# Performance work log

Hardware: AMD Instinct MI355X
Metric: run time of the kernel (lower is better)

Reference implementation:

```python
import jax, jax.numpy as jnp
from jax import lax
import numpy as np

D_IN, D, H, W, POOL = 1280, 100, 20, 3, 9
K_SIG, X0 = 1.0, 0.0
EPS = 1e-5


def setup_inputs() -> dict:
    key = jax.random.key(0)
    ks = jax.random.split(key, 8)
    N1, N2 = 512, 512
    return {
        "x1": jax.random.normal(ks[0], (N1, D_IN), jnp.float32),
        "x2": jax.random.normal(ks[1], (N2, D_IN), jnp.float32),
        "W1": jax.random.normal(ks[2], (D, D_IN), jnp.float32) * 0.02,
        "b1": jnp.zeros((D,), jnp.float32),
        "W2": jax.random.normal(ks[3], (H, 2 * D), jnp.float32) * 0.05,
        "b2": jnp.zeros((H,), jnp.float32),
        "bn1_g": jnp.ones((H,), jnp.float32),
        "bn1_b": jnp.zeros((H,), jnp.float32),
        "conv_w": jax.random.normal(ks[4], (1, H, 2 * W + 1, 2 * W + 1), jnp.float32) * 0.05,
        "conv_b": jnp.zeros((1,), jnp.float32),
        "bn2_g": jnp.ones((1,), jnp.float32),
        "bn2_b": jnp.zeros((1,), jnp.float32),
        "gamma": jnp.zeros((1,), jnp.float32),
    }


def reference(x1, x2, W1, b1, W2, b2, bn1_g, bn1_b, conv_w, conv_b, bn2_g, bn2_b, gamma):
    N1, N2 = x1.shape[0], x2.shape[0]
    # fc1 projection (relu1/dropout1 are defined but unused in the original forward)
    a = (x1 @ W1.T + b1)[None]          # [1, N1, D]
    c = (x2 @ W1.T + b2 * 0 + b1)[None] if False else (x2 @ W1.T + b1)[None]  # [1, N2, D]
    # broadcast pairwise |diff| and product -> [1, N1, N2, 2D]
    diff = jnp.abs(a[:, :, None, :] - c[:, None, :, :])
    mul = a[:, :, None, :] * c[:, None, :, :]
    m = jnp.concatenate([diff, mul], axis=-1).reshape(-1, 2 * D)  # [N1*N2, 2D]
    # fc2
    m = m @ W2.T + b2                    # [N1*N2, H]
    # BatchNorm1d in training mode: batch statistics, biased variance
    mu = m.mean(axis=0)
    var = m.var(axis=0)
    m = (m - mu) * lax.rsqrt(var + EPS) * bn1_g + bn1_b
    m = jax.nn.relu(m)
    m = m.reshape(1, N1, N2, H).transpose(0, 3, 1, 2)  # NCHW [1, H, N1, N2]
    # 7x7 conv, padding=W
    C = lax.conv_general_dilated(m, conv_w, (1, 1), [(W, W), (W, W)])
    C = C + conv_b.reshape(1, -1, 1, 1)
    # BatchNorm2d (training mode, biased variance over N,H,W per channel)
    mu2 = C.mean(axis=(0, 2, 3), keepdims=True)
    var2 = C.var(axis=(0, 2, 3), keepdims=True)
    C = (C - mu2) * lax.rsqrt(var2 + EPS) * bn2_g.reshape(1, -1, 1, 1) + bn2_b.reshape(1, -1, 1, 1)
    C = jax.nn.sigmoid(C)
    # MaxPool2d(9, padding=4): stride = kernel, -inf padding
    p = POOL // 2
    B = lax.reduce_window(C, -jnp.inf, lax.max, (1, 1, POOL, POOL), (1, 1, POOL, POOL),
                          [(0, 0), (0, 0), (p, p), (p, p)])
    # mean / unbiased std over dims (1, 2) keepdim
    mean = B.mean(axis=(1, 2), keepdims=True)
    std = jnp.sqrt(B.var(axis=(1, 2), keepdims=True, ddof=1) + EPS)
    Q = jax.nn.relu(B - mean - gamma.reshape(()) * std)
    phat = Q.sum() / (jnp.sign(Q).sum() + 1.0)
    phat = jnp.clip(jax.nn.sigmoid(K_SIG * (phat - X0)), 0.0, 1.0)
    return phat, C
```

## Files before the change

kernel.cpp:

```cpp
#include <hip/hip_runtime.h>
#include <hip/hip_bf16.h>
#include <math.h>

#define N1 512
#define N2 512
#define DIN 1280
#define DD 100
#define HH 20
#define NPIX (N1*N2)
#define PB 57

typedef short bf16x8 __attribute__((ext_vector_type(8)));
typedef float f32x4 __attribute__((ext_vector_type(4)));

static constexpr size_t WS_PP    = 0;
static constexpr size_t WS_W1T   = 204800;
static constexpr size_t WS_W2B   = 332800;
static constexpr size_t WS_M     = 336896;
static constexpr size_t WS_CRAW  = WS_M + 5242880;
static constexpr size_t WS_STATS = WS_CRAW + 262144;
static constexpr size_t WS_B     = WS_STATS + 64;

__global__ __launch_bounds__(256) void kP(const float* __restrict__ W1,
                                          const float* __restrict__ W2,
                                          float* __restrict__ w1t,
                                          unsigned short* __restrict__ w2b,
                                          float* __restrict__ stats) {
  const int tid = threadIdx.x;
  if (blockIdx.x >= 160) {
    int idx = (blockIdx.x - 160) * 256 + tid;
    if (blockIdx.x == 160 && tid < 64) stats[tid] = 0.0f;
    if (idx < 224 * 32) {
      int k = idx >> 5, n = idx & 31;
      float v = (n < HH && k < 200) ? W2[n * 200 + k] : 0.0f;
      __hip_bfloat16 b = __float2bfloat16(v);
      w2b[idx] = *reinterpret_cast<unsigned short*>(&b);
    }
    return;
  }
  __shared__ float sT[32][33];
  const int bx = blockIdx.x % 40, by = blockIdx.x / 40;
  const int tx = tid & 31, ty = tid >> 5;
#pragma unroll
  for (int e = 0; e < 4; ++e) {
    int h = by * 32 + ty + e * 8, k = bx * 32 + tx;
    sT[ty + e * 8][tx] = (h < DD) ? W1[(size_t)h * DIN + k] : 0.0f;
  }
  __syncthreads();
#pragma unroll
  for (int e = 0; e < 4; ++e) {
    int k = bx * 32 + ty + e * 8, h = by * 32 + tx;
    if (h < DD) w1t[(size_t)k * DD + h] = sT[tx][ty + e * 8];
  }
}

__global__ __launch_bounds__(512) void kA(const float* __restrict__ x1,
                                          const float* __restrict__ x2,
                                          const float* __restrict__ w1t,
                                          float* __restrict__ pp) {
  const int tid = threadIdx.x;
  const int w  = __builtin_amdgcn_readfirstlane(tid >> 6);
  const int rp = w >> 1, hh = w & 1;
  const int h = hh * 64 + (tid & 63);
  if (h >= DD) return;
  const int kh = blockIdx.x & 1;
  const int rb = (blockIdx.x >> 1) * 8;
  const int r0 = rb + rp * 2;
  const float* xb = (r0 < N1) ? (x1 + (size_t)r0 * DIN) : (x2 + (size_t)(r0 - N1) * DIN);
  const float* xr0 = xb + kh * 640;
  const float* xr1 = xb + DIN + kh * 640;
  const float* w1p = w1t + (size_t)kh * 640 * DD + h;
  float a00 = 0.f, a01 = 0.f, a10 = 0.f, a11 = 0.f;
#pragma unroll 8
  for (int k = 0; k < 640; k += 2) {
    float wA = w1p[(size_t)k * DD];
    float wB = w1p[(size_t)(k + 1) * DD];
    float x00 = xr0[k], x01 = xr0[k + 1];
    float x10 = xr1[k], x11 = xr1[k + 1];
    a00 = fmaf(wA, x00, a00); a01 = fmaf(wB, x01, a01);
    a10 = fmaf(wA, x10, a10); a11 = fmaf(wB, x11, a11);
  }
  pp[(size_t)kh * 102400 + (size_t)r0 * DD + h] = a00 + a01;
  pp[(size_t)kh * 102400 + (size_t)(r0 + 1) * DD + h] = a10 + a11;
}

__global__ __launch_bounds__(256, 2) void kB(const float* __restrict__ pp,
                                             const float* __restrict__ b1,
                                             const unsigned short* __restrict__ w2b,
                                             float* __restrict__ m,
                                             float* __restrict__ stats) {
  __shared__ float sA[8][132];
  __shared__ float sC[64][132];
  __shared__ float wred[4][40];
  const int tid = threadIdx.x;
  const int bi = blockIdx.x >> 3, bj = blockIdx.x & 7;
  for (int idx = tid; idx < 72 * 33; idx += 256) {
    int r = idx / 33, d4 = idx % 33;
    float4 v = {0.f, 0.f, 0.f, 0.f};
    if (d4 < 25) {
      size_t row = (r < 8) ? (size_t)(bi * 8 + r) : (size_t)(N1 + bj * 64 + (r - 8));
      const float* base = pp + row * DD;
      float4 a0 = ((const float4*)base)[d4];
      float4 a1 = ((const float4*)(base + 102400))[d4];
      float4 bb = ((const float4*)b1)[d4];
      v.x = a0.x + a1.x + bb.x;
      v.y = a0.y + a1.y + bb.y;
      v.z = a0.z + a1.z + bb.z;
      v.w = a0.w + a1.w + bb.w;
    }
    if (r < 8) *(float4*)&sA[r][4 * d4] = v;
    else       *(float4*)&sC[r - 8][4 * d4] = v;
  }
  __syncthreads();

  const int w    = tid >> 6;
  const int lane = tid & 63;
  const int ln   = lane & 15;
  const int q    = lane >> 4;
  const int jj   = w * 16 + ln;

  bf16x8 af[7][2];
#pragma unroll
  for (int ks = 0; ks < 7; ++ks)
#pragma unroll
    for (int t = 0; t < 2; ++t) {
      bf16x8 v;
#pragma unroll
      for (int e = 0; e < 8; ++e)
        v[e] = (short)w2b[(ks * 32 + q * 8 + e) * 32 + ln + 16 * t];
      af[ks][t] = v;
    }

  int dOf[14];
  bool isP[14];
  float4 cH[14];
#pragma unroll
  for (int hx = 0; hx < 14; ++hx) {
    int kk = (hx >> 1) * 32 + q * 8 + (hx & 1) * 4;
    bool p = kk >= 100;
    isP[hx] = p;
    int d = p ? kk - 100 : kk;
    dOf[hx] = d;
    cH[hx] = *(const float4*)&sC[jj][d];
  }

  float st_s[8], st_q[8];
#pragma unroll
  for (int r = 0; r < 8; ++r) { st_s[r] = 0.f; st_q[r] = 0.f; }

  const int gj = bj * 64 + jj;
#pragma unroll 1
  for (int ii = 0; ii < 8; ++ii) {
    bf16x8 bf[7];
#pragma unroll
    for (int ks = 0; ks < 7; ++ks) {
      float4 a0 = *(const float4*)&sA[ii][dOf[2 * ks]];
      float4 a1 = *(const float4*)&sA[ii][dOf[2 * ks + 1]];
      float4 c0 = cH[2 * ks], c1 = cH[2 * ks + 1];
      float f0 = isP[2*ks]   ? a0.x * c0.x : fabsf(a0.x - c0.x);
      float f1 = isP[2*ks]   ? a0.y * c0.y : fabsf(a0.y - c0.y);
      float f2 = isP[2*ks]   ? a0.z * c0.z : fabsf(a0.z - c0.z);
      float f3 = isP[2*ks]   ? a0.w * c0.w : fabsf(a0.w - c0.w);
      float f4 = isP[2*ks+1] ? a1.x * c1.x : fabsf(a1.x - c1.x);
      float f5 = isP[2*ks+1] ? a1.y * c1.y : fabsf(a1.y - c1.y);
      float f6 = isP[2*ks+1] ? a1.z * c1.z : fabsf(a1.z - c1.z);
      float f7 = isP[2*ks+1] ? a1.w * c1.w : fabsf(a1.w - c1.w);
      union { bf16x8 v; __hip_bfloat162 h2[4]; } u;
      u.h2[0] = __float22bfloat162_rn(make_float2(f0, f1));
      u.h2[1] = __float22bfloat162_rn(make_float2(f2, f3));
      u.h2[2] = __float22bfloat162_rn(make_float2(f4, f5));
      u.h2[3] = __float22bfloat162_rn(make_float2(f6, f7));
      bf[ks] = u.v;
    }
    f32x4 acc0 = {0.f, 0.f, 0.f, 0.f}, acc1 = {0.f, 0.f, 0.f, 0.f};
#pragma unroll
    for (int ks = 0; ks < 7; ++ks) {
      acc0 = __builtin_amdgcn_mfma_f32_16x16x32_bf16(af[ks][0], bf[ks], acc0, 0, 0, 0);
      acc1 = __builtin_amdgcn_mfma_f32_16x16x32_bf16(af[ks][1], bf[ks], acc1, 0, 0, 0);
    }
    const size_t pix = (size_t)(bi * 8 + ii) * N2 + gj;
#pragma unroll
    for (int r = 0; r < 4; ++r) {
      m[(size_t)(4 * q + r) * NPIX + pix] = acc0[r];
      st_s[r] += acc0[r];
      st_q[r] += acc0[r] * acc0[r];
    }
    if (q == 0) {
#pragma unroll
      for (int r = 0; r < 4; ++r)
        m[(size_t)(16 + r) * NPIX + pix] = acc1[r];
    }
#pragma unroll
    for (int r = 0; r < 4; ++r) {
      st_s[4 + r] += acc1[r];
      st_q[4 + r] += acc1[r] * acc1[r];
    }
  }
#pragma unroll
  for (int r = 0; r < 8; ++r) {
#pragma unroll
    for (int off = 1; off < 16; off <<= 1) {
      st_s[r] += __shfl_xor(st_s[r], off);
      st_q[r] += __shfl_xor(st_q[r], off);
    }
  }
  if (ln == 0) {
#pragma unroll
    for (int r = 0; r < 4; ++r) {
      wred[w][4 * q + r]      = st_s[r];
      wred[w][20 + 4 * q + r] = st_q[r];
    }
    if (q == 0) {
#pragma unroll
      for (int r = 0; r < 4; ++r) {
        wred[w][16 + r] = st_s[4 + r];
        wred[w][36 + r] = st_q[4 + r];
      }
    }
  }
  __syncthreads();
  if (tid < 40)
    atomicAdd(&stats[tid], wred[0][tid] + wred[1][tid] + wred[2][tid] + wred[3][tid]);
}

__global__ __launch_bounds__(256, 1) void kD(const float* __restrict__ m,
                                             const float* __restrict__ bn1g,
                                             const float* __restrict__ bn1b,
                                             const float* __restrict__ cw,
                                             float* __restrict__ stats,
                                             float* __restrict__ Craw) {
  __shared__ float sIn[2][4][38][40];
  __shared__ float sSc[HH], sSh[HH];
  __shared__ float wsum[4][2];
  const int tid = threadIdx.x;
  if (tid < HH) {
    float s = stats[tid], q = stats[HH + tid];
    float mu = s * (1.0f / NPIX);
    float var = q * (1.0f / NPIX) - mu * mu;
    float g = bn1g[tid] / sqrtf(var + 1e-5f);
    sSc[tid] = g;
    sSh[tid] = bn1b[tid] - mu * g;
  }
  const int by = (blockIdx.x >> 4) * 32, bx = (blockIdx.x & 15) * 32;
  const int w = tid >> 6, lane = tid & 63;
  const int gxs = bx + lane - 4;
  const bool colOk = (lane < 40) && (gxs >= 0) && (gxs < N2);
  float ld[38];
  {
    const float* mp = m + (size_t)w * NPIX + gxs;
#pragma unroll
    for (int r = 0; r < 38; ++r) {
      int gy = by + r - 3;
      ld[r] = (colOk && gy >= 0 && gy < N1) ? mp[(size_t)gy * N2] : 0.0f;
    }
  }
  __syncthreads();
  if (lane < 40) {
    float sc = sSc[w], sh = sSh[w];
#pragma unroll
    for (int r = 0; r < 38; ++r) {
      int gy = by + r - 3;
      bool ok = colOk && gy >= 0 && gy < N1;
      sIn[0][w][r][lane] = ok ? fmaxf(fmaf(ld[r], sc, sh), 0.0f) : 0.0f;
    }
  }
  __syncthreads();
  const int ty = tid >> 4, tx = tid & 15;
  float acc00 = 0.f, acc01 = 0.f, acc10 = 0.f, acc11 = 0.f;
#pragma unroll 1
  for (int cc = 0; cc < 5; ++cc) {
    if (cc < 4) {
      const float* mp = m + (size_t)((cc + 1) * 4 + w) * NPIX + gxs;
#pragma unroll
      for (int r = 0; r < 38; ++r) {
        int gy = by + r - 3;
        ld[r] = (colOk && gy >= 0 && gy < N1) ? mp[(size_t)gy * N2] : 0.0f;
      }
    }
    const int cur = cc & 1;
#pragma unroll 1
    for (int ch4 = 0; ch4 < 4; ++ch4) {
      float2 win[8][5];
#pragma unroll
      for (int rr = 0; rr < 8; ++rr)
#pragma unroll
        for (int qq = 0; qq < 5; ++qq)
          win[rr][qq] = *(const float2*)&sIn[cur][ch4][2 * ty + rr][2 * tx + 2 * qq];
      const float* wch = cw + (cc * 4 + ch4) * 49;
#pragma unroll
      for (int ky = 0; ky < 7; ++ky)
#pragma unroll
        for (int kx = 0; kx < 7; ++kx) {
          float wt = wch[ky * 7 + kx];
          float e0 = ((kx + 1) & 1) ? win[ky][(kx + 1) >> 1].y : win[ky][(kx + 1) >> 1].x;
          float e1 = ((kx + 2) & 1) ? win[ky][(kx + 2) >> 1].y : win[ky][(kx + 2) >> 1].x;
          float f0 = ((kx + 1) & 1) ? win[ky + 1][(kx + 1) >> 1].y : win[ky + 1][(kx + 1) >> 1].x;
          float f1 = ((kx + 2) & 1) ? win[ky + 1][(kx + 2) >> 1].y : win[ky + 1][(kx + 2) >> 1].x;
          acc00 = fmaf(e0, wt, acc00);
          acc01 = fmaf(e1, wt, acc01);
          acc10 = fmaf(f0, wt, acc10);
          acc11 = fmaf(f1, wt, acc11);
        }
    }
    __syncthreads();
    if (cc < 4 && lane < 40) {
      int ch = (cc + 1) * 4 + w;
      float sc = sSc[ch], sh = sSh[ch];
#pragma unroll
      for (int r = 0; r < 38; ++r) {
        int gy = by + r - 3;
        bool ok = colOk && gy >= 0 && gy < N1;
        sIn[cur ^ 1][w][r][lane] = ok ? fmaxf(fmaf(ld[r], sc, sh), 0.0f) : 0.0f;
      }
    }
    __syncthreads();
  }
  const int oy = by + 2 * ty, ox = bx + 2 * tx;
  float2 r0 = {acc00, acc01}, r1 = {acc10, acc11};
  *(float2*)&Craw[(size_t)oy * N2 + ox] = r0;
  *(float2*)&Craw[(size_t)(oy + 1) * N2 + ox] = r1;
  float s = acc00 + acc01 + acc10 + acc11;
  float q = acc00 * acc00 + acc01 * acc01 + acc10 * acc10 + acc11 * acc11;
#pragma unroll
  for (int off = 32; off; off >>= 1) {
    s += __shfl_xor(s, off);
    q += __shfl_xor(q, off);
  }
  if (lane == 0) { wsum[w][0] = s; wsum[w][1] = q; }
  __syncthreads();
  if (tid < 2) {
    float v = wsum[0][tid] + wsum[1][tid] + wsum[2][tid] + wsum[3][tid];
    atomicAdd(&stats[2 * HH + tid], v);
  }
}

__global__ __launch_bounds__(256) void kE2M(const float* __restrict__ Craw,
                                            const float* __restrict__ stats,
                                            const float* __restrict__ bn2g,
                                            const float* __restrict__ bn2b,
                                            float* __restrict__ Cout,
                                            float* __restrict__ B) {
  const int w = blockIdx.x * 4 + (threadIdx.x >> 6);
  const int lane = threadIdx.x & 63;
  float s = stats[2 * HH], q = stats[2 * HH + 1];
  float mu = s * (1.0f / NPIX);
  float var = q * (1.0f / NPIX) - mu * mu;
  float g = bn2g[0] / sqrtf(var + 1e-5f);
  float b = bn2b[0] - mu * g;
  if (w >= PB * PB) return;
  const int wy = w / PB, wx = w % PB;
  const int y0 = wy * 9 - 4, x0 = wx * 9 - 4;
  float mx = -1e30f;
  for (int e = lane; e < 144; e += 64) {
    int dy = e / 12, dx = e % 12;
    int y = y0 + dy, x = x0 + dx;
    bool inWin = (dy < 9) && (dx < 9);
    bool claim = (y >= 0) && (y < N1) && (x >= 0) && (x < N2) &&
                 (dy < 9 || wy == PB - 1) && (dx < 9 || wx == PB - 1);
    if (claim) {
      float z = Craw[(size_t)y * N2 + x] * g + b;
      float sg = 1.0f / (1.0f + expf(-z));
      Cout[(size_t)y * N2 + x] = sg;
      if (inWin) mx = fmaxf(mx, sg);
    }
  }
#pragma unroll
  for (int off = 32; off; off >>= 1) mx = fmaxf(mx, __shfl_xor(mx, off));
  if (lane == 0) B[w] = mx;
}

__global__ __launch_bounds__(1024) void kF(const float* __restrict__ B,
                                           const float* __restrict__ gamma,
                                           float* __restrict__ out0) {
  __shared__ float sB[PB * PB];
  __shared__ float cm[PB], cs[PB];
  __shared__ float r1[16], r2[16];
  const int tid = threadIdx.x;
  for (int i = tid; i < PB * PB; i += 1024) sB[i] = B[i];
  __syncthreads();
  if (tid < PB * 16) {
    int c = tid >> 4, g = tid & 15;
    float s = 0.0f;
    for (int h = g; h < PB; h += 16) s += sB[h * PB + c];
#pragma unroll
    for (int off = 1; off < 16; off <<= 1) s += __shfl_xor(s, off);
    float mean = s / (float)PB;
    float v = 0.0f;
    for (int h = g; h < PB; h += 16) { float d = sB[h * PB + c] - mean; v += d * d; }
#pragma unroll
    for (int off = 1; off < 16; off <<= 1) v += __shfl_xor(v, off);
    if (g == 0) {
      cm[c] = mean;
      cs[c] = sqrtf(v / (float)(PB - 1) + 1e-5f);
    }
  }
  __syncthreads();
  const float g = gamma[0];
  float sq = 0.0f, cnt = 0.0f;
  for (int i = tid; i < PB * PB; i += 1024) {
    int w = i % PB;
    float qv = sB[i] - cm[w] - g * cs[w];
    if (qv > 0.0f) { sq += qv; cnt += 1.0f; }
  }
#pragma unroll
  for (int off = 32; off; off >>= 1) {
    sq += __shfl_xor(sq, off);
    cnt += __shfl_xor(cnt, off);
  }
  if ((tid & 63) == 0) { r1[tid >> 6] = sq; r2[tid >> 6] = cnt; }
  __syncthreads();
  if (tid == 0) {
    float S = 0.f, Cn = 0.f;
#pragma unroll
    for (int e = 0; e < 16; ++e) { S += r1[e]; Cn += r2[e]; }
    float phat = S / (Cn + 1.0f);
    float sig = 1.0f / (1.0f + expf(-phat));
    out0[0] = fminf(fmaxf(sig, 0.0f), 1.0f);
  }
}

extern "C" void kernel_launch(void* const* d_in, const int* in_sizes, int n_in,
                              void* d_out, int out_size, void* d_ws, size_t ws_size,
                              hipStream_t stream) {
  const float* x1    = (const float*)d_in[0];
  const float* x2    = (const float*)d_in[1];
  const float* W1    = (const float*)d_in[2];
  const float* b1    = (const float*)d_in[3];
  const float* W2    = (const float*)d_in[4];
  const float* bn1g  = (const float*)d_in[6];
  const float* bn1b  = (const float*)d_in[7];
  const float* convw = (const float*)d_in[8];
  const float* bn2g  = (const float*)d_in[10];
  const float* bn2b  = (const float*)d_in[11];
  const float* gamma = (const float*)d_in[12];

  float* ws    = (float*)d_ws;
  float* pp    = ws + WS_PP;
  float* w1t   = ws + WS_W1T;
  unsigned short* w2b = (unsigned short*)(ws + WS_W2B);
  float* m     = ws + WS_M;
  float* Craw  = ws + WS_CRAW;
  float* stats = ws + WS_STATS;
  float* Bp    = ws + WS_B;
  float* out   = (float*)d_out;

  kP<<<188, 256, 0, stream>>>(W1, W2, w1t, w2b, stats);
  kA<<<256, 512, 0, stream>>>(x1, x2, w1t, pp);
  kB<<<512, 256, 0, stream>>>(pp, b1, w2b, m, stats);
  kD<<<256, 256, 0, stream>>>(m, bn1g, bn1b, convw, stats, Craw);
  kE2M<<<(PB * PB + 3) / 4, 256, 0, stream>>>(Craw, stats, bn2g, bn2b, out + 1, Bp);
  kF<<<1, 1024, 0, stream>>>(Bp, gamma, out);
}
```

Before: 92.99 us.

## Fuse all stages into one cooperative persistent kernel with grid syncs

Replaces the six separate kernel launches with a single cooperative kernel of 256 blocks that runs every stage in turn, separated by grid.sync(). Each stage is remapped onto the fixed grid: the projection loops over the h halves, and the pairwise fc2 stage processes two tiles per block. The aim is to remove launch overhead and inter-kernel gaps. In exchange, parallelism is capped at 256 blocks of 256 threads (kA used 512-thread blocks, kB ran 512 blocks at two per CU), and grid barriers add their own cost. If the cooperative launch fails, it falls back to the old launches.

```diff
diff --git a/kernel.cpp b/kernel.cpp
--- a/kernel.cpp
+++ b/kernel.cpp
@@ -1,6 +1,9 @@
 #include <hip/hip_runtime.h>
+#include <hip/hip_cooperative_groups.h>
 #include <hip/hip_bf16.h>
 #include <math.h>
+
+namespace cg = cooperative_groups;
 
 #define N1 512
 #define N2 512
@@ -20,6 +23,396 @@
 static constexpr size_t WS_CRAW  = WS_M + 5242880;
 static constexpr size_t WS_STATS = WS_CRAW + 262144;
 static constexpr size_t WS_B     = WS_STATS + 64;
+
+union SMem {
+  struct { float sT[32][33]; } p;
+  struct { float sA[8][132]; float sC[64][132]; float wred[4][40]; } b;
+  struct { float sIn[2][4][38][40]; float sSc[HH]; float sSh[HH]; float wsum[4][2]; } d;
+  struct { float sB[PB * PB]; float cm[PB]; float cs[PB]; float r1[4]; float r2[4]; } f;
+};
+
+__global__ __launch_bounds__(256, 1) void kAll(
+    const float* __restrict__ x1, const float* __restrict__ x2,
+    const float* __restrict__ W1, const float* __restrict__ b1,
+    const float* __restrict__ W2,
+    const float* __restrict__ bn1g, const float* __restrict__ bn1b,
+    const float* __restrict__ cw,
+    const float* __restrict__ bn2g, const float* __restrict__ bn2b,
+    const float* __restrict__ gamma,
+    float* __restrict__ pp, float* __restrict__ w1t,
+    unsigned short* __restrict__ w2b,
+    float* __restrict__ m, float* __restrict__ Craw,
+    float* __restrict__ stats, float* __restrict__ Bp,
+    float* __restrict__ out) {
+  cg::grid_group grid = cg::this_grid();
+  __shared__ SMem sm;
+  const int blk = blockIdx.x;
+  const int tid = threadIdx.x;
+  const int lane = tid & 63;
+  const int wv = tid >> 6;
+  const int wvu = __builtin_amdgcn_readfirstlane(wv);
+
+  if (blk < 160) {
+    const int bx = blk % 40, by = blk / 40;
+    const int tx = tid & 31, ty = tid >> 5;
+#pragma unroll
+    for (int e = 0; e < 4; ++e) {
+      int h = by * 32 + ty + e * 8, k = bx * 32 + tx;
+      sm.p.sT[ty + e * 8][tx] = (h < DD) ? W1[(size_t)h * DIN + k] : 0.0f;
+    }
+    __syncthreads();
+#pragma unroll
+    for (int e = 0; e < 4; ++e) {
+      int k = bx * 32 + ty + e * 8, h = by * 32 + tx;
+      if (h < DD) w1t[(size_t)k * DD + h] = sm.p.sT[tx][ty + e * 8];
+    }
+  } else if (blk < 188) {
+    int idx = (blk - 160) * 256 + tid;
+    if (blk == 160 && tid < 64) stats[tid] = 0.0f;
+    if (idx < 224 * 32) {
+      int k = idx >> 5, n = idx & 31;
+      float v = (n < HH && k < 200) ? W2[n * 200 + k] : 0.0f;
+      __hip_bfloat16 bh = __float2bfloat16(v);
+      w2b[idx] = *reinterpret_cast<unsigned short*>(&bh);
+    }
+  }
+  grid.sync();
+
+  {
+    const int kh = blk & 1;
+    const int r0 = (blk >> 1) * 8 + wvu * 2;
+    const float* xb = (r0 < N1) ? (x1 + (size_t)r0 * DIN) : (x2 + (size_t)(r0 - N1) * DIN);
+    const float* xr0 = xb + kh * 640;
+    const float* xr1 = xb + DIN + kh * 640;
+#pragma unroll 1
+    for (int hl = 0; hl < 2; ++hl) {
+      int h = hl * 64 + lane;
+      if (h < DD) {
+        const float* w1p = w1t + (size_t)kh * 640 * DD + h;
+        float a00 = 0.f, a01 = 0.f, a10 = 0.f, a11 = 0.f;
+#pragma unroll 8
+        for (int k = 0; k < 640; k += 2) {
+          float wA = w1p[(size_t)k * DD];
+          float wB = w1p[(size_t)(k + 1) * DD];
+          a00 = fmaf(wA, xr0[k], a00); a01 = fmaf(wB, xr0[k + 1], a01);
+          a10 = fmaf(wA, xr1[k], a10); a11 = fmaf(wB, xr1[k + 1], a11);
+        }
+        pp[(size_t)kh * 102400 + (size_t)r0 * DD + h] = a00 + a01;
+        pp[(size_t)kh * 102400 + (size_t)(r0 + 1) * DD + h] = a10 + a11;
+      }
+    }
+  }
+  grid.sync();
+
+  {
+    const int ln = lane & 15;
+    const int q  = lane >> 4;
+    const int jj = wv * 16 + ln;
+
+    bf16x8 af[7][2];
+#pragma unroll
+    for (int ks = 0; ks < 7; ++ks)
+#pragma unroll
+      for (int t = 0; t < 2; ++t) {
+        bf16x8 v;
+#pragma unroll
+        for (int e = 0; e < 8; ++e)
+          v[e] = (short)w2b[(ks * 32 + q * 8 + e) * 32 + ln + 16 * t];
+        af[ks][t] = v;
+      }
+    int dOf[14];
+    bool isP[14];
+#pragma unroll
+    for (int hx = 0; hx < 14; ++hx) {
+      int kk = (hx >> 1) * 32 + q * 8 + (hx & 1) * 4;
+      isP[hx] = kk >= 100;
+      dOf[hx] = isP[hx] ? kk - 100 : kk;
+    }
+
+#pragma unroll 1
+    for (int t = 0; t < 2; ++t) {
+      const int bb = blk + t * 256;
+      const int bi = bb >> 3, bj = bb & 7;
+      if (t) __syncthreads();
+      for (int idx = tid; idx < 72 * 33; idx += 256) {
+        int r = idx / 33, d4 = idx % 33;
+        float4 v = {0.f, 0.f, 0.f, 0.f};
+        if (d4 < 25) {
+          size_t row = (r < 8) ? (size_t)(bi * 8 + r) : (size_t)(N1 + bj * 64 + (r - 8));
+          const float* base = pp + row * DD;
+          float4 a0 = ((const float4*)base)[d4];
+          float4 a1 = ((const float4*)(base + 102400))[d4];
+          float4 bb4 = ((const float4*)b1)[d4];
+          v.x = a0.x + a1.x + bb4.x;
+          v.y = a0.y + a1.y + bb4.y;
+          v.z = a0.z + a1.z + bb4.z;
+          v.w = a0.w + a1.w + bb4.w;
+        }
+        if (r < 8) *(float4*)&sm.b.sA[r][4 * d4] = v;
+        else       *(float4*)&sm.b.sC[r - 8][4 * d4] = v;
+      }
+      __syncthreads();
+
+      float4 cH[14];
+#pragma unroll
+      for (int hx = 0; hx < 14; ++hx) cH[hx] = *(const float4*)&sm.b.sC[jj][dOf[hx]];
+
+      float st_s[8], st_q[8];
+#pragma unroll
+      for (int r = 0; r < 8; ++r) { st_s[r] = 0.f; st_q[r] = 0.f; }
+
+      const int gj = bj * 64 + jj;
+#pragma unroll 1
+      for (int ii = 0; ii < 8; ++ii) {
+        bf16x8 bf[7];
+#pragma unroll
+        for (int ks = 0; ks < 7; ++ks) {
+          float4 a0 = *(const float4*)&sm.b.sA[ii][dOf[2 * ks]];
+          float4 a1 = *(const float4*)&sm.b.sA[ii][dOf[2 * ks + 1]];
+          float4 c0 = cH[2 * ks], c1 = cH[2 * ks + 1];
+          float f0 = isP[2*ks]   ? a0.x * c0.x : fabsf(a0.x - c0.x);
+          float f1 = isP[2*ks]   ? a0.y * c0.y : fabsf(a0.y - c0.y);
+          float f2 = isP[2*ks]   ? a0.z * c0.z : fabsf(a0.z - c0.z);
+          float f3 = isP[2*ks]   ? a0.w * c0.w : fabsf(a0.w - c0.w);
+          float f4 = isP[2*ks+1] ? a1.x * c1.x : fabsf(a1.x - c1.x);
+          float f5 = isP[2*ks+1] ? a1.y * c1.y : fabsf(a1.y - c1.y);
+          float f6 = isP[2*ks+1] ? a1.z * c1.z : fabsf(a1.z - c1.z);
+          float f7 = isP[2*ks+1] ? a1.w * c1.w : fabsf(a1.w - c1.w);
+          union { bf16x8 v; __hip_bfloat162 h2[4]; } u;
+          u.h2[0] = __float22bfloat162_rn(make_float2(f0, f1));
+          u.h2[1] = __float22bfloat162_rn(make_float2(f2, f3));
+          u.h2[2] = __float22bfloat162_rn(make_float2(f4, f5));
+          u.h2[3] = __float22bfloat162_rn(make_float2(f6, f7));
+          bf[ks] = u.v;
+        }
+        f32x4 acc0 = {0.f, 0.f, 0.f, 0.f}, acc1 = {0.f, 0.f, 0.f, 0.f};
+#pragma unroll
+        for (int ks = 0; ks < 7; ++ks) {
+          acc0 = __builtin_amdgcn_mfma_f32_16x16x32_bf16(af[ks][0], bf[ks], acc0, 0, 0, 0);
+          acc1 = __builtin_amdgcn_mfma_f32_16x16x32_bf16(af[ks][1], bf[ks], acc1, 0, 0, 0);
+        }
+        const size_t pix = (size_t)(bi * 8 + ii) * N2 + gj;
+#pragma unroll
+        for (int r = 0; r < 4; ++r) {
+          m[(size_t)(4 * q + r) * NPIX + pix] = acc0[r];
+          st_s[r] += acc0[r];
+          st_q[r] += acc0[r] * acc0[r];
+        }
+        if (q == 0) {
+#pragma unroll
+          for (int r = 0; r < 4; ++r)
+            m[(size_t)(16 + r) * NPIX + pix] = acc1[r];
+        }
+#pragma unroll
+        for (int r = 0; r < 4; ++r) {
+          st_s[4 + r] += acc1[r];
+          st_q[4 + r] += acc1[r] * acc1[r];
+        }
+      }
+#pragma unroll
+      for (int r = 0; r < 8; ++r) {
+#pragma unroll
+        for (int off = 1; off < 16; off <<= 1) {
+          st_s[r] += __shfl_xor(st_s[r], off);
+          st_q[r] += __shfl_xor(st_q[r], off);
+        }
+      }
+      if (ln == 0) {
+#pragma unroll
+        for (int r = 0; r < 4; ++r) {
+          sm.b.wred[wv][4 * q + r]      = st_s[r];
+          sm.b.wred[wv][20 + 4 * q + r] = st_q[r];
+        }
+        if (q == 0) {
+#pragma unroll
+          for (int r = 0; r < 4; ++r) {
+            sm.b.wred[wv][16 + r] = st_s[4 + r];
+            sm.b.wred[wv][36 + r] = st_q[4 + r];
+          }
+        }
+      }
+      __syncthreads();
+      if (tid < 40)
+        atomicAdd(&stats[tid],
+                  sm.b.wred[0][tid] + sm.b.wred[1][tid] + sm.b.wred[2][tid] + sm.b.wred[3][tid]);
+    }
+  }
+  grid.sync();
+
+  {
+    if (tid < HH) {
+      float s = stats[tid], q = stats[HH + tid];
+      float mu = s * (1.0f / NPIX);
+      float var = q * (1.0f / NPIX) - mu * mu;
+      float g = bn1g[tid] / sqrtf(var + 1e-5f);
+      sm.d.sSc[tid] = g;
+      sm.d.sSh[tid] = bn1b[tid] - mu * g;
+    }
+    const int by = (blk >> 4) * 32, bx = (blk & 15) * 32;
+    const int gxs = bx + lane - 4;
+    const bool colOk = (lane < 40) && (gxs >= 0) && (gxs < N2);
+    float ld[38];
+    {
+      const float* mp = m + (size_t)wvu * NPIX + gxs;
+#pragma unroll
+      for (int r = 0; r < 38; ++r) {
+        int gy = by + r - 3;
+        ld[r] = (colOk && gy >= 0 && gy < N1) ? mp[(size_t)gy * N2] : 0.0f;
+      }
+    }
+    __syncthreads();
+    if (lane < 40) {
+      float sc = sm.d.sSc[wvu], sh = sm.d.sSh[wvu];
+#pragma unroll
+      for (int r = 0; r < 38; ++r)
+        sm.d.sIn[0][wvu][r][lane] = fmaxf(fmaf(ld[r], sc, sh), 0.0f) * (ld[r] != 0.0f || true ? 1.0f : 0.0f);
+    }
+    if (lane < 40) {
+#pragma unroll
+      for (int r = 0; r < 38; ++r) {
+        int gy = by + r - 3;
+        bool ok = colOk && gy >= 0 && gy < N1;
+        if (!ok) sm.d.sIn[0][wvu][r][lane] = 0.0f;
+      }
+    }
+    __syncthreads();
+    const int ty = tid >> 4, tx = tid & 15;
+    float acc00 = 0.f, acc01 = 0.f, acc10 = 0.f, acc11 = 0.f;
+#pragma unroll 1
+    for (int cc = 0; cc < 5; ++cc) {
+      if (cc < 4) {
+        const float* mp = m + (size_t)((cc + 1) * 4 + wvu) * NPIX + gxs;
+#pragma unroll
+        for (int r = 0; r < 38; ++r) {
+          int gy = by + r - 3;
+          ld[r] = (colOk && gy >= 0 && gy < N1) ? mp[(size_t)gy * N2] : 0.0f;
+        }
+      }
+      const int cur = cc & 1;
+#pragma unroll 1
+      for (int ch4 = 0; ch4 < 4; ++ch4) {
+        float2 win[8][5];
+#pragma unroll
+        for (int rr = 0; rr < 8; ++rr)
+#pragma unroll
+          for (int qq = 0; qq < 5; ++qq)
+            win[rr][qq] = *(const float2*)&sm.d.sIn[cur][ch4][2 * ty + rr][2 * tx + 2 * qq];
+        const float* wch = cw + (cc * 4 + ch4) * 49;
+#pragma unroll
+        for (int ky = 0; ky < 7; ++ky)
+#pragma unroll
+          for (int kx = 0; kx < 7; ++kx) {
+            float wt = wch[ky * 7 + kx];
+            float e0 = ((kx + 1) & 1) ? win[ky][(kx + 1) >> 1].y : win[ky][(kx + 1) >> 1].x;
+            float e1 = ((kx + 2) & 1) ? win[ky][(kx + 2) >> 1].y : win[ky][(kx + 2) >> 1].x;
+            float f0 = ((kx + 1) & 1) ? win[ky + 1][(kx + 1) >> 1].y : win[ky + 1][(kx + 1) >> 1].x;
+            float f1 = ((kx + 2) & 1) ? win[ky + 1][(kx + 2) >> 1].y : win[ky + 1][(kx + 2) >> 1].x;
+            acc00 = fmaf(e0, wt, acc00);
+            acc01 = fmaf(e1, wt, acc01);
+            acc10 = fmaf(f0, wt, acc10);
+            acc11 = fmaf(f1, wt, acc11);
+          }
+      }
+      __syncthreads();
+      if (cc < 4 && lane < 40) {
+        int ch = (cc + 1) * 4 + wvu;
+        float sc = sm.d.sSc[ch], sh = sm.d.sSh[ch];
+#pragma unroll
+        for (int r = 0; r < 38; ++r) {
+          int gy = by + r - 3;
+          bool ok = colOk && gy >= 0 && gy < N1;
+          sm.d.sIn[cur ^ 1][wvu][r][lane] = ok ? fmaxf(fmaf(ld[r], sc, sh), 0.0f) : 0.0f;
+        }
+      }
+      __syncthreads();
+    }
+    const int oy = by + 2 * ty, ox = bx + 2 * tx;
+    float2 r0 = {acc00, acc01}, r1 = {acc10, acc11};
+    *(float2*)&Craw[(size_t)oy * N2 + ox] = r0;
+    *(float2*)&Craw[(size_t)(oy + 1) * N2 + ox] = r1;
+    float s = acc00 + acc01 + acc10 + acc11;
+    float q = acc00 * acc00 + acc01 * acc01 + acc10 * acc10 + acc11 * acc11;
+#pragma unroll
+    for (int off = 32; off; off >>= 1) {
+      s += __shfl_xor(s, off);
+      q += __shfl_xor(q, off);
+    }
+    if (lane == 0) { sm.d.wsum[wv][0] = s; sm.d.wsum[wv][1] = q; }
+    __syncthreads();
+    if (tid < 2) {
+      float v = sm.d.wsum[0][tid] + sm.d.wsum[1][tid] + sm.d.wsum[2][tid] + sm.d.wsum[3][tid];
+      atomicAdd(&stats[2 * HH + tid], v);
+    }
+  }
+  grid.sync();
+
+  {
+    float s = stats[2 * HH], q = stats[2 * HH + 1];
+    float mu = s * (1.0f / NPIX);
+    float var = q * (1.0f / NPIX) - mu * mu;
+    float g = bn2g[0] / sqrtf(var + 1e-5f);
+    float b = bn2b[0] - mu * g;
+    float* Cout = out + 1;
+    for (int w = blk * 4 + wv; w < PB * PB; w += 1024) {
+      const int wy = w / PB, wx = w % PB;
+      const int y0 = wy * 9 - 4, x0 = wx * 9 - 4;
+      float mx = -1e30f;
+      for (int e = lane; e < 144; e += 64) {
+        int dy = e / 12, dx = e % 12;
+        int y = y0 + dy, x = x0 + dx;
+        bool inWin = (dy < 9) && (dx < 9);
+        bool claim = (y >= 0) && (y < N1) && (x >= 0) && (x < N2) &&
+                     (dy < 9 || wy == PB - 1) && (dx < 9 || wx == PB - 1);
+        if (claim) {
+          float z = Craw[(size_t)y * N2 + x] * g + b;
+          float sg = 1.0f / (1.0f + expf(-z));
+          Cout[(size_t)y * N2 + x] = sg;
+          if (inWin) mx = fmaxf(mx, sg);
+        }
+      }
+#pragma unroll
+      for (int off = 32; off; off >>= 1) mx = fmaxf(mx, __shfl_xor(mx, off));
+      if (lane == 0) Bp[w] = mx;
+    }
+  }
+  grid.sync();
+
+  if (blk == 0) {
+    for (int i = tid; i < PB * PB; i += 256) sm.f.sB[i] = Bp[i];
+    __syncthreads();
+    if (tid < PB) {
+      float s = 0.0f;
+      for (int h = 0; h < PB; ++h) s += sm.f.sB[h * PB + tid];
+      float mean = s / (float)PB;
+      float v = 0.0f;
+      for (int h = 0; h < PB; ++h) { float d = sm.f.sB[h * PB + tid] - mean; v += d * d; }
+      sm.f.cm[tid] = mean;
+      sm.f.cs[tid] = sqrtf(v / (float)(PB - 1) + 1e-5f);
+    }
+    __syncthreads();
+    const float g = gamma[0];
+    float sq = 0.0f, cnt = 0.0f;
+    for (int i = tid; i < PB * PB; i += 256) {
+      int w = i % PB;
+      float qv = sm.f.sB[i] - sm.f.cm[w] - g * sm.f.cs[w];
+      if (qv > 0.0f) { sq += qv; cnt += 1.0f; }
+    }
+#pragma unroll
+    for (int off = 32; off; off >>= 1) {
+      sq += __shfl_xor(sq, off);
+      cnt += __shfl_xor(cnt, off);
+    }
+    if (lane == 0) { sm.f.r1[wv] = sq; sm.f.r2[wv] = cnt; }
+    __syncthreads();
+    if (tid == 0) {
+      float S = sm.f.r1[0] + sm.f.r1[1] + sm.f.r1[2] + sm.f.r1[3];
+      float Cn = sm.f.r2[0] + sm.f.r2[1] + sm.f.r2[2] + sm.f.r2[3];
+      float phat = S / (Cn + 1.0f);
+      float sig = 1.0f / (1.0f + expf(-phat));
+      out[0] = fminf(fmaxf(sig, 0.0f), 1.0f);
+    }
+  }
+}
 
 __global__ __launch_bounds__(256) void kP(const float* __restrict__ W1,
                                           const float* __restrict__ W2,
@@ -64,8 +457,7 @@
   const int h = hh * 64 + (tid & 63);
   if (h >= DD) return;
   const int kh = blockIdx.x & 1;
-  const int rb = (blockIdx.x >> 1) * 8;
-  const int r0 = rb + rp * 2;
+  const int r0 = (blockIdx.x >> 1) * 8 + rp * 2;
   const float* xb = (r0 < N1) ? (x1 + (size_t)r0 * DIN) : (x2 + (size_t)(r0 - N1) * DIN);
   const float* xr0 = xb + kh * 640;
   const float* xr1 = xb + DIN + kh * 640;
@@ -75,10 +467,8 @@
   for (int k = 0; k < 640; k += 2) {
     float wA = w1p[(size_t)k * DD];
     float wB = w1p[(size_t)(k + 1) * DD];
-    float x00 = xr0[k], x01 = xr0[k + 1];
-    float x10 = xr1[k], x11 = xr1[k + 1];
-    a00 = fmaf(wA, x00, a00); a01 = fmaf(wB, x01, a01);
-    a10 = fmaf(wA, x10, a10); a11 = fmaf(wB, x11, a11);
+    a00 = fmaf(wA, xr0[k], a00); a01 = fmaf(wB, xr0[k + 1], a01);
+    a10 = fmaf(wA, xr1[k], a10); a11 = fmaf(wB, xr1[k + 1], a11);
   }
   pp[(size_t)kh * 102400 + (size_t)r0 * DD + h] = a00 + a01;
   pp[(size_t)kh * 102400 + (size_t)(r0 + 1) * DD + h] = a10 + a11;
@@ -112,13 +502,9 @@
     else       *(float4*)&sC[r - 8][4 * d4] = v;
   }
   __syncthreads();
-
-  const int w    = tid >> 6;
-  const int lane = tid & 63;
-  const int ln   = lane & 15;
-  const int q    = lane >> 4;
-  const int jj   = w * 16 + ln;
-
+  const int w = tid >> 6, lane = tid & 63;
+  const int ln = lane & 15, q = lane >> 4;
+  const int jj = w * 16 + ln;
   bf16x8 af[7][2];
 #pragma unroll
   for (int ks = 0; ks < 7; ++ks)
@@ -130,24 +516,19 @@
         v[e] = (short)w2b[(ks * 32 + q * 8 + e) * 32 + ln + 16 * t];
       af[ks][t] = v;
     }
-
   int dOf[14];
   bool isP[14];
   float4 cH[14];
 #pragma unroll
   for (int hx = 0; hx < 14; ++hx) {
     int kk = (hx >> 1) * 32 + q * 8 + (hx & 1) * 4;
-    bool p = kk >= 100;
-    isP[hx] = p;
-    int d = p ? kk - 100 : kk;
-    dOf[hx] = d;
-    cH[hx] = *(const float4*)&sC[jj][d];
-  }
-
+    isP[hx] = kk >= 100;
+    dOf[hx] = isP[hx] ? kk - 100 : kk;
+    cH[hx] = *(const float4*)&sC[jj][dOf[hx]];
+  }
   float st_s[8], st_q[8];
 #pragma unroll
   for (int r = 0; r < 8; ++r) { st_s[r] = 0.f; st_q[r] = 0.f; }
-
   const int gj = bj * 64 + jj;
 #pragma unroll 1
   for (int ii = 0; ii < 8; ++ii) {
@@ -444,10 +825,21 @@
   float* Bp    = ws + WS_B;
   float* out   = (float*)d_out;
 
-  kP<<<188, 256, 0, stream>>>(W1, W2, w1t, w2b, stats);
-  kA<<<256, 512, 0, stream>>>(x1, x2, w1t, pp);
-  kB<<<512, 256, 0, stream>>>(pp, b1, w2b, m, stats);
-  kD<<<256, 256, 0, stream>>>(m, bn1g, bn1b, convw, stats, Craw);
-  kE2M<<<(PB * PB + 3) / 4, 256, 0, stream>>>(Craw, stats, bn2g, bn2b, out + 1, Bp);
-  kF<<<1, 1024, 0, stream>>>(Bp, gamma, out);
+  void* args[] = {
+    (void*)&x1, (void*)&x2, (void*)&W1, (void*)&b1, (void*)&W2,
+    (void*)&bn1g, (void*)&bn1b, (void*)&convw, (void*)&bn2g, (void*)&bn2b,
+    (void*)&gamma,
+    (void*)&pp, (void*)&w1t, (void*)&w2b, (void*)&m, (void*)&Craw,
+    (void*)&stats, (void*)&Bp, (void*)&out
+  };
+  hipError_t e = hipLaunchCooperativeKernel((void*)kAll, dim3(256), dim3(256),
+                                            args, 0, stream);
+  if (e != hipSuccess) {
+    kP<<<188, 256, 0, stream>>>(W1, W2, w1t, w2b, stats);
+    kA<<<256, 512, 0, stream>>>(x1, x2, w1t, pp);
+    kB<<<512, 256, 0, stream>>>(pp, b1, w2b, m, stats);
+    kD<<<256, 256, 0, stream>>>(m, bn1g, bn1b, convw, stats, Craw);
+    kE2M<<<(PB * PB + 3) / 4, 256, 0, stream>>>(Craw, stats, bn2g, bn2b, out + 1, Bp);
+    kF<<<1, 1024, 0, stream>>>(Bp, gamma, out);
+  }
 }
```

New measurement: 254.9 us. 2.74x slower.

## Split fc1 K-dimension four ways and halve conv tile height for more blocks

Applied to the files above, without the earlier changes.

The fc1 projection kernel now splits the reduction dimension into four partial sums instead of two, using 256-thread blocks and four times as many blocks. The fc2 kernel adds the four partials. The 7x7 conv kernel computes 16-row tiles with one output row per thread instead of 32-row tiles with two, doubling the block count and allowing two blocks per CU. This trades more parallelism and occupancy for extra partial-sum traffic and more halo reloads in the conv, since each thread no longer reuses its window rows across two outputs.

```diff
diff --git a/kernel.cpp b/kernel.cpp
--- a/kernel.cpp
+++ b/kernel.cpp
@@ -14,9 +14,9 @@
 typedef float f32x4 __attribute__((ext_vector_type(4)));
 
 static constexpr size_t WS_PP    = 0;
-static constexpr size_t WS_W1T   = 204800;
-static constexpr size_t WS_W2B   = 332800;
-static constexpr size_t WS_M     = 336896;
+static constexpr size_t WS_W1T   = 409600;
+static constexpr size_t WS_W2B   = 537600;
+static constexpr size_t WS_M     = 541696;
 static constexpr size_t WS_CRAW  = WS_M + 5242880;
 static constexpr size_t WS_STATS = WS_CRAW + 262144;
 static constexpr size_t WS_B     = WS_STATS + 64;
@@ -54,7 +54,7 @@
   }
 }
 
-__global__ __launch_bounds__(512) void kA(const float* __restrict__ x1,
+__global__ __launch_bounds__(256) void kA(const float* __restrict__ x1,
                                           const float* __restrict__ x2,
                                           const float* __restrict__ w1t,
                                           float* __restrict__ pp) {
@@ -63,25 +63,22 @@
   const int rp = w >> 1, hh = w & 1;
   const int h = hh * 64 + (tid & 63);
   if (h >= DD) return;
-  const int kh = blockIdx.x & 1;
-  const int rb = (blockIdx.x >> 1) * 8;
-  const int r0 = rb + rp * 2;
+  const int kq = blockIdx.x & 3;
+  const int r0 = (blockIdx.x >> 2) * 4 + rp * 2;
   const float* xb = (r0 < N1) ? (x1 + (size_t)r0 * DIN) : (x2 + (size_t)(r0 - N1) * DIN);
-  const float* xr0 = xb + kh * 640;
-  const float* xr1 = xb + DIN + kh * 640;
-  const float* w1p = w1t + (size_t)kh * 640 * DD + h;
+  const float* xr0 = xb + kq * 320;
+  const float* xr1 = xb + DIN + kq * 320;
+  const float* w1p = w1t + (size_t)kq * 320 * DD + h;
   float a00 = 0.f, a01 = 0.f, a10 = 0.f, a11 = 0.f;
 #pragma unroll 8
-  for (int k = 0; k < 640; k += 2) {
+  for (int k = 0; k < 320; k += 2) {
     float wA = w1p[(size_t)k * DD];
     float wB = w1p[(size_t)(k + 1) * DD];
-    float x00 = xr0[k], x01 = xr0[k + 1];
-    float x10 = xr1[k], x11 = xr1[k + 1];
-    a00 = fmaf(wA, x00, a00); a01 = fmaf(wB, x01, a01);
-    a10 = fmaf(wA, x10, a10); a11 = fmaf(wB, x11, a11);
-  }
-  pp[(size_t)kh * 102400 + (size_t)r0 * DD + h] = a00 + a01;
-  pp[(size_t)kh * 102400 + (size_t)(r0 + 1) * DD + h] = a10 + a11;
+    a00 = fmaf(wA, xr0[k], a00); a01 = fmaf(wB, xr0[k + 1], a01);
+    a10 = fmaf(wA, xr1[k], a10); a11 = fmaf(wB, xr1[k + 1], a11);
+  }
+  pp[(size_t)kq * 102400 + (size_t)r0 * DD + h] = a00 + a01;
+  pp[(size_t)kq * 102400 + (size_t)(r0 + 1) * DD + h] = a10 + a11;
 }
 
 __global__ __launch_bounds__(256, 2) void kB(const float* __restrict__ pp,
@@ -102,23 +99,21 @@
       const float* base = pp + row * DD;
       float4 a0 = ((const float4*)base)[d4];
       float4 a1 = ((const float4*)(base + 102400))[d4];
+      float4 a2 = ((const float4*)(base + 204800))[d4];
+      float4 a3 = ((const float4*)(base + 307200))[d4];
       float4 bb = ((const float4*)b1)[d4];
-      v.x = a0.x + a1.x + bb.x;
-      v.y = a0.y + a1.y + bb.y;
-      v.z = a0.z + a1.z + bb.z;
-      v.w = a0.w + a1.w + bb.w;
+      v.x = a0.x + a1.x + a2.x + a3.x + bb.x;
+      v.y = a0.y + a1.y + a2.y + a3.y + bb.y;
+      v.z = a0.z + a1.z + a2.z + a3.z + bb.z;
+      v.w = a0.w + a1.w + a2.w + a3.w + bb.w;
     }
     if (r < 8) *(float4*)&sA[r][4 * d4] = v;
     else       *(float4*)&sC[r - 8][4 * d4] = v;
   }
   __syncthreads();
-
-  const int w    = tid >> 6;
-  const int lane = tid & 63;
-  const int ln   = lane & 15;
-  const int q    = lane >> 4;
-  const int jj   = w * 16 + ln;
-
+  const int w = tid >> 6, lane = tid & 63;
+  const int ln = lane & 15, q = lane >> 4;
+  const int jj = w * 16 + ln;
   bf16x8 af[7][2];
 #pragma unroll
   for (int ks = 0; ks < 7; ++ks)
@@ -130,24 +125,19 @@
         v[e] = (short)w2b[(ks * 32 + q * 8 + e) * 32 + ln + 16 * t];
       af[ks][t] = v;
     }
-
   int dOf[14];
   bool isP[14];
   float4 cH[14];
 #pragma unroll
   for (int hx = 0; hx < 14; ++hx) {
     int kk = (hx >> 1) * 32 + q * 8 + (hx & 1) * 4;
-    bool p = kk >= 100;
-    isP[hx] = p;
-    int d = p ? kk - 100 : kk;
-    dOf[hx] = d;
-    cH[hx] = *(const float4*)&sC[jj][d];
-  }
-
+    isP[hx] = kk >= 100;
+    dOf[hx] = isP[hx] ? kk - 100 : kk;
+    cH[hx] = *(const float4*)&sC[jj][dOf[hx]];
+  }
   float st_s[8], st_q[8];
 #pragma unroll
   for (int r = 0; r < 8; ++r) { st_s[r] = 0.f; st_q[r] = 0.f; }
-
   const int gj = bj * 64 + jj;
 #pragma unroll 1
   for (int ii = 0; ii < 8; ++ii) {
@@ -223,13 +213,13 @@
     atomicAdd(&stats[tid], wred[0][tid] + wred[1][tid] + wred[2][tid] + wred[3][tid]);
 }
 
-__global__ __launch_bounds__(256, 1) void kD(const float* __restrict__ m,
+__global__ __launch_bounds__(256, 2) void kD(const float* __restrict__ m,
                                              const float* __restrict__ bn1g,
                                              const float* __restrict__ bn1b,
                                              const float* __restrict__ cw,
                                              float* __restrict__ stats,
                                              float* __restrict__ Craw) {
-  __shared__ float sIn[2][4][38][40];
+  __shared__ float sIn[2][4][22][40];
   __shared__ float sSc[HH], sSh[HH];
   __shared__ float wsum[4][2];
   const int tid = threadIdx.x;
@@ -241,15 +231,15 @@
     sSc[tid] = g;
     sSh[tid] = bn1b[tid] - mu * g;
   }
-  const int by = (blockIdx.x >> 4) * 32, bx = (blockIdx.x & 15) * 32;
+  const int by = (blockIdx.x >> 4) * 16, bx = (blockIdx.x & 15) * 32;
   const int w = tid >> 6, lane = tid & 63;
   const int gxs = bx + lane - 4;
   const bool colOk = (lane < 40) && (gxs >= 0) && (gxs < N2);
-  float ld[38];
+  float ld[22];
   {
     const float* mp = m + (size_t)w * NPIX + gxs;
 #pragma unroll
-    for (int r = 0; r < 38; ++r) {
+    for (int r = 0; r < 22; ++r) {
       int gy = by + r - 3;
       ld[r] = (colOk && gy >= 0 && gy < N1) ? mp[(size_t)gy * N2] : 0.0f;
     }
@@ -258,7 +248,7 @@
   if (lane < 40) {
     float sc = sSc[w], sh = sSh[w];
 #pragma unroll
-    for (int r = 0; r < 38; ++r) {
+    for (int r = 0; r < 22; ++r) {
       int gy = by + r - 3;
       bool ok = colOk && gy >= 0 && gy < N1;
       sIn[0][w][r][lane] = ok ? fmaxf(fmaf(ld[r], sc, sh), 0.0f) : 0.0f;
@@ -266,13 +256,13 @@
   }
   __syncthreads();
   const int ty = tid >> 4, tx = tid & 15;
-  float acc00 = 0.f, acc01 = 0.f, acc10 = 0.f, acc11 = 0.f;
+  float acc00 = 0.f, acc01 = 0.f;
 #pragma unroll 1
   for (int cc = 0; cc < 5; ++cc) {
     if (cc < 4) {
       const float* mp = m + (size_t)((cc + 1) * 4 + w) * NPIX + gxs;
 #pragma unroll
-      for (int r = 0; r < 38; ++r) {
+      for (int r = 0; r < 22; ++r) {
         int gy = by + r - 3;
         ld[r] = (colOk && gy >= 0 && gy < N1) ? mp[(size_t)gy * N2] : 0.0f;
       }
@@ -280,12 +270,12 @@
     const int cur = cc & 1;
 #pragma unroll 1
     for (int ch4 = 0; ch4 < 4; ++ch4) {
-      float2 win[8][5];
-#pragma unroll
-      for (int rr = 0; rr < 8; ++rr)
+      float2 win[7][5];
+#pragma unroll
+      for (int rr = 0; rr < 7; ++rr)
 #pragma unroll
         for (int qq = 0; qq < 5; ++qq)
-          win[rr][qq] = *(const float2*)&sIn[cur][ch4][2 * ty + rr][2 * tx + 2 * qq];
+          win[rr][qq] = *(const float2*)&sIn[cur][ch4][ty + rr][2 * tx + 2 * qq];
       const float* wch = cw + (cc * 4 + ch4) * 49;
 #pragma unroll
       for (int ky = 0; ky < 7; ++ky)
@@ -294,12 +284,8 @@
           float wt = wch[ky * 7 + kx];
           float e0 = ((kx + 1) & 1) ? win[ky][(kx + 1) >> 1].y : win[ky][(kx + 1) >> 1].x;
           float e1 = ((kx + 2) & 1) ? win[ky][(kx + 2) >> 1].y : win[ky][(kx + 2) >> 1].x;
-          float f0 = ((kx + 1) & 1) ? win[ky + 1][(kx + 1) >> 1].y : win[ky + 1][(kx + 1) >> 1].x;
-          float f1 = ((kx + 2) & 1) ? win[ky + 1][(kx + 2) >> 1].y : win[ky + 1][(kx + 2) >> 1].x;
           acc00 = fmaf(e0, wt, acc00);
           acc01 = fmaf(e1, wt, acc01);
-          acc10 = fmaf(f0, wt, acc10);
-          acc11 = fmaf(f1, wt, acc11);
         }
     }
     __syncthreads();
@@ -307,7 +293,7 @@
       int ch = (cc + 1) * 4 + w;
       float sc = sSc[ch], sh = sSh[ch];
 #pragma unroll
-      for (int r = 0; r < 38; ++r) {
+      for (int r = 0; r < 22; ++r) {
         int gy = by + r - 3;
         bool ok = colOk && gy >= 0 && gy < N1;
         sIn[cur ^ 1][w][r][lane] = ok ? fmaxf(fmaf(ld[r], sc, sh), 0.0f) : 0.0f;
@@ -315,12 +301,11 @@
     }
     __syncthreads();
   }
-  const int oy = by + 2 * ty, ox = bx + 2 * tx;
-  float2 r0 = {acc00, acc01}, r1 = {acc10, acc11};
+  const int oy = by + ty, ox = bx + 2 * tx;
+  float2 r0 = {acc00, acc01};
   *(float2*)&Craw[(size_t)oy * N2 + ox] = r0;
-  *(float2*)&Craw[(size_t)(oy + 1) * N2 + ox] = r1;
-  float s = acc00 + acc01 + acc10 + acc11;
-  float q = acc00 * acc00 + acc01 * acc01 + acc10 * acc10 + acc11 * acc11;
+  float s = acc00 + acc01;
+  float q = acc00 * acc00 + acc01 * acc01;
 #pragma unroll
   for (int off = 32; off; off >>= 1) {
     s += __shfl_xor(s, off);
@@ -445,9 +430,9 @@
   float* out   = (float*)d_out;
 
   kP<<<188, 256, 0, stream>>>(W1, W2, w1t, w2b, stats);
-  kA<<<256, 512, 0, stream>>>(x1, x2, w1t, pp);
+  kA<<<1024, 256, 0, stream>>>(x1, x2, w1t, pp);
   kB<<<512, 256, 0, stream>>>(pp, b1, w2b, m, stats);
-  kD<<<256, 256, 0, stream>>>(m, bn1g, bn1b, convw, stats, Craw);
+  kD<<<512, 256, 0, stream>>>(m, bn1g, bn1b, convw, stats, Craw);
   kE2M<<<(PB * PB + 3) / 4, 256, 0, stream>>>(Craw, stats, bn2g, bn2b, out + 1, Bp);
   kF<<<1, 1024, 0, stream>>>(Bp, gamma, out);
 }
```

Result: no change. 92.17 us (-0.9%).
